# Kernel tuning notes

Measured on AMD Instinct MI355X. Metric: run time of the kernel, lower is better.

The kernel has to match this reference:

```python
import jax, jax.numpy as jnp
import numpy as np

B, S, D = 8, 1024, 1024
H, DK = 16, 64  # heads, key_size (== head_size)
NEG = 1e12


def setup_inputs() -> dict:
    key = jax.random.key(0)
    ks = jax.random.split(key, 10)
    s = 1.0 / np.sqrt(D)
    return {
        "q": jax.random.normal(ks[0], (B, S, D), jnp.float32),
        "k": jax.random.normal(ks[1], (B, S, D), jnp.float32),
        "v": jax.random.normal(ks[2], (B, S, D), jnp.float32),
        "pos_bias": jax.random.normal(ks[3], (S, S, DK), jnp.float32) * 0.02,
        "Wq": jax.random.normal(ks[4], (D, H * DK), jnp.float32) * s,
        "Wk": jax.random.normal(ks[5], (D, H * DK), jnp.float32) * s,
        "Wv": jax.random.normal(ks[6], (D, H * DK), jnp.float32) * s,
        "Wo": jax.random.normal(ks[7], (H * DK, D), jnp.float32) * s,
        "bq": jnp.zeros((H * DK,), jnp.float32),
        "bk": jnp.zeros((H * DK,), jnp.float32),
        "bv": jnp.zeros((H * DK,), jnp.float32),
        "bo": jnp.zeros((D,), jnp.float32),
        "q_mask": jnp.ones((B, S), jnp.int32),
        "v_mask": jnp.ones((B, S), jnp.int32),
    }


def reference(q, k, v, pos_bias, Wq, Wk, Wv, Wo, bq, bk, bv, bo, q_mask, v_mask):
    qm = q_mask.astype(q.dtype)  # [B,Sq]
    vm = v_mask.astype(q.dtype)  # [B,Sk]
    # Projections (faithful quirk: K is projected from v, as in the source)
    qw = (q @ Wq + bq).reshape(B, S, H, DK)
    kw = (v @ Wk + bk).reshape(B, S, H, DK)
    vw = (v @ Wv + bv).reshape(B, S, H, DK)
    # scores + inline relative-position bias ('typial_relative' branch)
    a = jnp.einsum('bjhd,bkhd->bhjk', qw, kw)
    a = a + jnp.einsum('bjhd,jkd->bhjk', qw, pos_bias)
    a = a / jnp.sqrt(jnp.asarray(DK, a.dtype))
    # additive key mask, then softmax over keys
    a = a - (1.0 - vm)[:, None, None, :] * NEG
    a = jax.nn.softmax(a, axis=-1)
    o = jnp.einsum('bhjk,bkhd->bjhd', a, vw)  # [B,Sq,H,DK]
    o = o.reshape(B, S, H * DK) @ Wo + bo
    # multiplicative query mask on output
    o = o * qm[:, :, None]
    return o
```

## Files before the change

kernel.cpp:

```cpp
#include <hip/hip_runtime.h>

using short8 = __attribute__((ext_vector_type(8))) short;
using f32x4  = __attribute__((ext_vector_type(4))) float;
using u16x4  = __attribute__((ext_vector_type(4))) unsigned short;
using fl4    = __attribute__((ext_vector_type(4))) float;

#define MFMA16(a, b, c) __builtin_amdgcn_mfma_f32_16x16x32_bf16((a), (b), (c), 0, 0, 0)

static __device__ __forceinline__ unsigned short f2bf(float f) {
  union { float f; unsigned u; } x; x.f = f;
  return (unsigned short)((x.u + 0x7FFFu + ((x.u >> 16) & 1u)) >> 16);
}
static __device__ __forceinline__ float bf2f(unsigned short s) {
  union { unsigned u; float f; } x; x.u = ((unsigned)s) << 16;
  return x.f;
}
static __device__ __forceinline__ float fexp2(float x) {
  float r; asm("v_exp_f32 %0, %1" : "=v"(r) : "v"(x)); return r;
}
static __device__ __forceinline__ unsigned pk2(float lo, float hi) {
  unsigned r; asm("v_cvt_pk_bf16_f32 %0, %1, %2" : "=v"(r) : "v"(lo), "v"(hi));
  return r;
}

static __device__ __forceinline__ void gload16(const void* g, void* l) {
  __builtin_amdgcn_global_load_lds((const __attribute__((address_space(1))) void*)g,
                                   (__attribute__((address_space(3))) void*)l, 16, 0, 0);
}

#define LOG2E 1.4426950408889634f

__global__ __launch_bounds__(256) void k_wconv4(
    const float* __restrict__ W0, const float* __restrict__ W1,
    const float* __restrict__ W2, const float* __restrict__ W3,
    unsigned short* __restrict__ Wt0, unsigned short* __restrict__ Wt1,
    unsigned short* __restrict__ Wt2, unsigned short* __restrict__ Wt3) {
  const float* W = (blockIdx.z == 0) ? W0 : (blockIdx.z == 1) ? W1
                   : (blockIdx.z == 2) ? W2 : W3;
  unsigned short* Wt = (blockIdx.z == 0) ? Wt0 : (blockIdx.z == 1) ? Wt1
                       : (blockIdx.z == 2) ? Wt2 : Wt3;
  __shared__ float tile[64][65];
  const int t = threadIdx.x;
  const int n0 = blockIdx.x * 64, k0 = blockIdx.y * 64;
#pragma unroll
  for (int p = 0; p < 4; ++p) {
    int row = p * 16 + (t >> 4);
    int c4 = (t & 15) * 4;
    fl4 val = *(const fl4*)&W[(size_t)(k0 + row) * 1024 + n0 + c4];
    tile[row][c4 + 0] = val[0];
    tile[row][c4 + 1] = val[1];
    tile[row][c4 + 2] = val[2];
    tile[row][c4 + 3] = val[3];
  }
  __syncthreads();
#pragma unroll
  for (int p = 0; p < 4; ++p) {
    int n = p * 16 + (t >> 4);
    int k4 = (t & 15) * 4;
    u16x4 u;
    u[0] = f2bf(tile[k4 + 0][n]);
    u[1] = f2bf(tile[k4 + 1][n]);
    u[2] = f2bf(tile[k4 + 2][n]);
    u[3] = f2bf(tile[k4 + 3][n]);
    *(u16x4*)&Wt[(size_t)(n0 + n) * 1024 + k0 + k4] = u;
  }
}

__global__ __launch_bounds__(256) void k_cvt(const float* __restrict__ a,
                                             const float* __restrict__ b,
                                             unsigned short* __restrict__ oa,
                                             unsigned short* __restrict__ ob) {
  const float* src = blockIdx.y ? b : a;
  unsigned short* dst = blockIdx.y ? ob : oa;
  size_t i = ((size_t)blockIdx.x * 256 + threadIdx.x) * 8;
  fl4 v0 = *(const fl4*)&src[i];
  fl4 v1 = *(const fl4*)&src[i + 4];
  u16x4 u0, u1;
  u0[0] = f2bf(v0[0]); u0[1] = f2bf(v0[1]); u0[2] = f2bf(v0[2]); u0[3] = f2bf(v0[3]);
  u1[0] = f2bf(v1[0]); u1[1] = f2bf(v1[1]); u1[2] = f2bf(v1[2]); u1[3] = f2bf(v1[3]);
  *(u16x4*)&dst[i] = u0;
  *(u16x4*)&dst[i + 4] = u1;
}

#define GEMM3_CORE(APTR, BPTR)                                                  \
  const int t = threadIdx.x, lane = t & 63, w = t >> 6;                         \
  const int g = lane >> 4, ln = lane & 15;                                      \
  const int wm = w >> 1, wn = w & 1;                                            \
  __shared__ unsigned short sh[24576];    \
  const int srow = lane >> 2;                                                   \
  const int sc = (lane & 3) ^ ((lane >> 3) & 3);                                \
  const int rsw = ((ln >> 1) & 3);                                              \
  f32x4 acc[4][4] = {};                                                         \
  _Pragma("unroll") for (int pre = 0; pre < 2; ++pre) {                         \
    _Pragma("unroll") for (int p = 0; p < 2; ++p) {                             \
      gload16(&APTR[(size_t)(m0 + p * 64 + w * 16 + srow) * 1024 + pre * 32 + sc * 8], \
              &sh[pre * 8192 + (p * 64 + w * 16) * 32]);                        \
      gload16(&BPTR[(size_t)(n0 + p * 64 + w * 16 + srow) * 1024 + pre * 32 + sc * 8], \
              &sh[pre * 8192 + 4096 + (p * 64 + w * 16) * 32]);                 \
    }                                                                           \
  }                                                                             \
  int cur = 0;                                                                  \
  for (int tt = 0; tt < 32; ++tt) {                                             \
    if (tt < 31) {                                                              \
      asm volatile("s_waitcnt vmcnt(4)" ::: "memory");                          \
    } else {                                                                    \
      asm volatile("s_waitcnt vmcnt(0)" ::: "memory");                          \
    }                                                                           \
    __builtin_amdgcn_sched_barrier(0);                                          \
    __builtin_amdgcn_s_barrier();                                               \
    __builtin_amdgcn_sched_barrier(0);                                          \
    if (tt < 30) {                                                              \
      int bb = cur + 2; if (bb >= 3) bb -= 3;                                   \
      int kk = (tt + 2) * 32;                                                   \
      _Pragma("unroll") for (int p = 0; p < 2; ++p) {                           \
        gload16(&APTR[(size_t)(m0 + p * 64 + w * 16 + srow) * 1024 + kk + sc * 8], \
                &sh[bb * 8192 + (p * 64 + w * 16) * 32]);                       \
        gload16(&BPTR[(size_t)(n0 + p * 64 + w * 16 + srow) * 1024 + kk + sc * 8], \
                &sh[bb * 8192 + 4096 + (p * 64 + w * 16) * 32]);                \
      }                                                                         \
    }                                                                           \
    const unsigned short* As = &sh[cur * 8192];                                 \
    const unsigned short* Bs = As + 4096;                                       \
    short8 af[4], bfr[4];                                                       \
    _Pragma("unroll") for (int fm = 0; fm < 4; ++fm)                            \
        af[fm] = *(const short8*)&As[(wm * 64 + fm * 16 + ln) * 32 + (g ^ rsw) * 8]; \
    _Pragma("unroll") for (int fn = 0; fn < 4; ++fn)                            \
        bfr[fn] = *(const short8*)&Bs[(wn * 64 + fn * 16 + ln) * 32 + (g ^ rsw) * 8]; \
    _Pragma("unroll") for (int fn = 0; fn < 4; ++fn) {                          \
      _Pragma("unroll") for (int fm = 0; fm < 4; ++fm)                          \
          acc[fm][fn] = MFMA16(af[fm], bfr[fn], acc[fm][fn]);                   \
    }                                                                           \
    cur = (cur == 2) ? 0 : cur + 1;                                             \
  }

__global__ __launch_bounds__(256) void k_proj3(
    const unsigned short* __restrict__ QB, const unsigned short* __restrict__ VB,
    const unsigned short* __restrict__ WtQ, const unsigned short* __restrict__ WtK,
    const unsigned short* __restrict__ WtV,
    const float* __restrict__ bq, const float* __restrict__ bk,
    const float* __restrict__ bv,
    unsigned short* __restrict__ QW, unsigned short* __restrict__ KW,
    unsigned short* __restrict__ VWT) {
  const int mode = blockIdx.z;
  const unsigned short* A8 = (mode == 0) ? QB : VB;
  const unsigned short* Wt = (mode == 0) ? WtQ : (mode == 1) ? WtK : WtV;
  const float* bias = (mode == 0) ? bq : (mode == 1) ? bk : bv;
  const int n0 = blockIdx.x * 128, m0 = blockIdx.y * 128;
  GEMM3_CORE(A8, Wt)
  __syncthreads();
  const float scale = (mode == 0) ? (0.125f * LOG2E) : 1.0f;
#pragma unroll
  for (int fn = 0; fn < 4; ++fn) {
    float bn = bias[n0 + wn * 64 + fn * 16 + ln];
#pragma unroll
    for (int fm = 0; fm < 4; ++fm) {
#pragma unroll
      for (int r = 0; r < 4; ++r) {
        float val = (acc[fm][fn][r] + bn) * scale;
        sh[(wm * 64 + fm * 16 + 4 * g + r) * 132 + wn * 64 + fn * 16 + ln] = f2bf(val);
      }
    }
  }
  __syncthreads();
  if (mode < 2) {
    unsigned short* OUT = (mode == 0) ? QW : KW;
#pragma unroll
    for (int p = 0; p < 16; ++p) {
      int row = p * 8 + (t >> 5), c4 = (t & 31) * 4;
      *(u16x4*)&OUT[(size_t)(m0 + row) * 1024 + n0 + c4] =
          *(const u16x4*)&sh[row * 132 + c4];
    }
  } else {
    const int b = m0 >> 10, s0 = m0 & 1023;
#pragma unroll
    for (int p = 0; p < 16; ++p) {
#pragma unroll
      for (int qh = 0; qh < 2; ++qh) {
        int hdl = p * 8 + (t >> 5);
        int sl = qh * 64 + (t & 31) * 2;
        unsigned lo = sh[sl * 132 + hdl];
        unsigned hi = sh[(sl + 1) * 132 + hdl];
        int hd = n0 + hdl;
        int h = hd >> 6, d = hd & 63;
        *(unsigned*)&VWT[((size_t)(b * 16 + h) * 64 + d) * 1024 + s0 + sl] =
            lo | (hi << 16);
      }
    }
  }
}

__global__ __launch_bounds__(256) void k_out3(
    const unsigned short* __restrict__ OB, const unsigned short* __restrict__ WtO,
    const float* __restrict__ bo, const int* __restrict__ qmask,
    float* __restrict__ out) {
  const int n0 = blockIdx.x * 128, m0 = blockIdx.y * 128;
  GEMM3_CORE(OB, WtO)
  float bn[4];
#pragma unroll
  for (int fn = 0; fn < 4; ++fn) bn[fn] = bo[n0 + wn * 64 + fn * 16 + ln];
#pragma unroll
  for (int fm = 0; fm < 4; ++fm) {
#pragma unroll
    for (int r = 0; r < 4; ++r) {
      int row = m0 + wm * 64 + fm * 16 + 4 * g + r;
      float qm = (float)qmask[row];
#pragma unroll
      for (int fn = 0; fn < 4; ++fn)
        out[(size_t)row * 1024 + n0 + wn * 64 + fn * 16 + ln] =
            (acc[fm][fn][r] + bn[fn]) * qm;
    }
  }
}

__global__ __launch_bounds__(256) void k_pbias(
    const unsigned short* __restrict__ QW, const float* __restrict__ pb,
    const int* __restrict__ vmask, unsigned short* __restrict__ CB, int jbase) {
  const int kt = blockIdx.x;
  const int jl = blockIdx.y;
  const int j = jbase + jl;
  const int t = threadIdx.x, lane = t & 63, w = t >> 6;
  const int g = lane >> 4, ln = lane & 15;
  const int wm = w >> 1, wn = w & 1;
  __shared__ unsigned short sm[18432];
  unsigned short* a_lds = sm;
  unsigned short* b_lds = sm + 9216;
#pragma unroll
  for (int p = 0; p < 8; ++p) {
    int i4 = p * 256 + t;
    int row = i4 >> 4, c4 = (i4 & 15) * 4;
    *(u16x4*)&a_lds[row * 72 + c4] =
        *(const u16x4*)&QW[((size_t)(row >> 4) * 1024 + j) * 1024 + (row & 15) * 64 + c4];
  }
#pragma unroll
  for (int p = 0; p < 8; ++p) {
    int i4 = p * 256 + t;
    int row = i4 >> 4, c4 = (i4 & 15) * 4;
    fl4 val = *(const fl4*)&pb[((size_t)j * 1024 + kt * 128 + row) * 64 + c4];
    u16x4 u;
    u[0] = f2bf(val[0]); u[1] = f2bf(val[1]);
    u[2] = f2bf(val[2]); u[3] = f2bf(val[3]);
    *(u16x4*)&b_lds[row * 72 + c4] = u;
  }
  __syncthreads();
  f32x4 acc[4][4] = {};
#pragma unroll
  for (int ks = 0; ks < 2; ++ks) {
    short8 af[4];
#pragma unroll
    for (int fm = 0; fm < 4; ++fm)
      af[fm] = *(const short8*)&a_lds[(wm * 64 + fm * 16 + ln) * 72 + ks * 32 + 8 * g];
#pragma unroll
    for (int fn = 0; fn < 4; ++fn) {
      short8 bfr = *(const short8*)&b_lds[(wn * 64 + fn * 16 + ln) * 72 + ks * 32 + 8 * g];
#pragma unroll
      for (int fm = 0; fm < 4; ++fm) acc[fm][fn] = MFMA16(af[fm], bfr, acc[fm][fn]);
    }
  }
  __syncthreads();
#pragma unroll
  for (int fn = 0; fn < 4; ++fn) {
    int kcol = kt * 128 + wn * 64 + fn * 16 + ln;
#pragma unroll
    for (int fm = 0; fm < 4; ++fm) {
      float off = vmask[(wm * 4 + fm) * 1024 + kcol] ? 0.f : (-1e12f * LOG2E);
#pragma unroll
      for (int r = 0; r < 4; ++r)
        sm[(wm * 64 + fm * 16 + 4 * g + r) * 132 + wn * 64 + fn * 16 + ln] =
            f2bf(acc[fm][fn][r] + off);
    }
  }
  __syncthreads();
#pragma unroll
  for (int p = 0; p < 16; ++p) {
    int row = p * 8 + (t >> 5), c4 = (t & 31) * 4;
    *(u16x4*)&CB[((size_t)row * 512 + jl) * 1024 + kt * 128 + c4] =
        *(const u16x4*)&sm[row * 132 + c4];
  }
}

__global__ __launch_bounds__(256) void k_attn(
    const unsigned short* __restrict__ QW, const unsigned short* __restrict__ KW,
    const unsigned short* __restrict__ VWT, const unsigned short* __restrict__ CB,
    unsigned short* __restrict__ OB, int jbase) {
  const int B = blockIdx.x;
  const int wrk = (B & 7) * 128 + (B >> 3);
  const int jt = wrk & 7, h = (wrk >> 3) & 15, b = wrk >> 7;
  const int t = threadIdx.x, lane = t & 63, w = t >> 6;
  const int g = lane >> 4, ln = lane & 15;
  const int j0 = jbase + jt * 64;
  const int jl0 = jt * 64;
  __shared__ unsigned short lds_k[128 * 72];
  __shared__ unsigned short lds_vt[64 * 136];
  __shared__ unsigned short lds_p[4 * 16 * 136];
  unsigned short* pw = &lds_p[w * (16 * 136)];
  short8 qf[2];
  {
    const size_t qrow = ((size_t)b * 1024 + (j0 + w * 16 + ln)) * 1024 + h * 64;
    qf[0] = *(const short8*)&QW[qrow + 8 * g];
    qf[1] = *(const short8*)&QW[qrow + 32 + 8 * g];
  }
  const size_t cb_row = ((size_t)(b * 16 + h) * 512 + jl0 + w * 16 + ln) * 1024;

  u16x4 rk[8], rv[8], rcb[8];
#define LOAD_KV(kt_)                                                              \
  {                                                                               \
    _Pragma("unroll") for (int p = 0; p < 8; ++p) {                               \
      int i4 = p * 256 + t;                                                       \
      int row = i4 >> 4, c4 = (i4 & 15) * 4;                                      \
      rk[p] = *(const u16x4*)&KW[((size_t)b * 1024 + (kt_) * 128 + row) * 1024 +  \
                                 h * 64 + c4];                                    \
    }                                                                             \
    _Pragma("unroll") for (int p = 0; p < 8; ++p) {                               \
      int i4 = p * 256 + t;                                                       \
      int row = i4 >> 5, c4 = (i4 & 31) * 4;                                      \
      rv[p] = *(const u16x4*)&VWT[(((size_t)b * 16 + h) * 64 + row) * 1024 +      \
                                  (kt_) * 128 + c4];                              \
    }                                                                             \
    _Pragma("unroll") for (int p = 0; p < 8; ++p)                                 \
        rcb[p] = *(const u16x4*)&CB[cb_row + (kt_) * 128 + p * 16 + 4 * g];       \
  }

  LOAD_KV(0);
  f32x4 o_acc[4] = {};
  float l_par = 0.f;

  for (int kt = 0; kt < 8; ++kt) {
    __syncthreads();
#pragma unroll
    for (int p = 0; p < 8; ++p) {
      int i4 = p * 256 + t;
      int row = i4 >> 4, c4 = (i4 & 15) * 4;
      *(u16x4*)&lds_k[row * 72 + c4] = rk[p];
    }
#pragma unroll
    for (int p = 0; p < 8; ++p) {
      int i4 = p * 256 + t;
      int row = i4 >> 5, c4 = (i4 & 31) * 4;
      *(u16x4*)&lds_vt[row * 136 + c4] = rv[p];
    }
    f32x4 s[8];
#pragma unroll
    for (int fm = 0; fm < 8; ++fm) {
#pragma unroll
      for (int r = 0; r < 4; ++r) s[fm][r] = bf2f(rcb[fm][r]);
    }
    if (kt < 7) LOAD_KV(kt + 1);
    __syncthreads();
#pragma unroll
    for (int ks = 0; ks < 2; ++ks) {
#pragma unroll
      for (int fm = 0; fm < 8; ++fm) {
        short8 af = *(const short8*)&lds_k[(fm * 16 + ln) * 72 + ks * 32 + 8 * g];
        s[fm] = MFMA16(af, qf[ks], s[fm]);
      }
    }
#pragma unroll
    for (int fm = 0; fm < 8; ++fm) {
      float pv0 = fexp2(s[fm][0] - 17.0f);
      float pv1 = fexp2(s[fm][1] - 17.0f);
      float pv2 = fexp2(s[fm][2] - 17.0f);
      float pv3 = fexp2(s[fm][3] - 17.0f);
      l_par += (pv0 + pv1) + (pv2 + pv3);
      union { u16x4 v; unsigned u[2]; } pp;
      pp.u[0] = pk2(pv0, pv1);
      pp.u[1] = pk2(pv2, pv3);
      *(u16x4*)&pw[ln * 136 + fm * 16 + 4 * g] = pp.v;
    }
    asm volatile("s_waitcnt lgkmcnt(0)" ::: "memory");
#pragma unroll
    for (int ks = 0; ks < 4; ++ks) {
      short8 bp = *(const short8*)&pw[ln * 136 + ks * 32 + 8 * g];
#pragma unroll
      for (int fm = 0; fm < 4; ++fm) {
        short8 av = *(const short8*)&lds_vt[(fm * 16 + ln) * 136 + ks * 32 + 8 * g];
        o_acc[fm] = MFMA16(av, bp, o_acc[fm]);
      }
    }
  }
  l_par += __shfl_xor(l_par, 16);
  l_par += __shfl_xor(l_par, 32);
  float inv = 1.0f / l_par;
  const size_t orow = ((size_t)b * 1024 + (j0 + w * 16 + ln)) * 1024 + h * 64;
#pragma unroll
  for (int fm = 0; fm < 4; ++fm) {
    union { u16x4 v; unsigned u[2]; } uo;
    uo.u[0] = pk2(o_acc[fm][0] * inv, o_acc[fm][1] * inv);
    uo.u[1] = pk2(o_acc[fm][2] * inv, o_acc[fm][3] * inv);
    *(u16x4*)&OB[orow + fm * 16 + 4 * g] = uo.v;
  }
#undef LOAD_KV
}

extern "C" void kernel_launch(void* const* d_in, const int* in_sizes, int n_in,
                              void* d_out, int out_size, void* d_ws, size_t ws_size,
                              hipStream_t stream) {
  const float* q  = (const float*)d_in[0];
  const float* v  = (const float*)d_in[2];
  const float* pb = (const float*)d_in[3];
  const float* Wq = (const float*)d_in[4];
  const float* Wk = (const float*)d_in[5];
  const float* Wv = (const float*)d_in[6];
  const float* Wo = (const float*)d_in[7];
  const float* bq = (const float*)d_in[8];
  const float* bk = (const float*)d_in[9];
  const float* bv = (const float*)d_in[10];
  const float* bo = (const float*)d_in[11];
  const int* qm = (const int*)d_in[12];
  const int* vm = (const int*)d_in[13];
  float* out = (float*)d_out;

  unsigned short* ws = (unsigned short*)d_ws;
  const size_t M1 = 1024 * 1024;
  unsigned short* WTQ = ws;
  unsigned short* WTK = WTQ + M1;
  unsigned short* WTV = WTK + M1;
  unsigned short* WTO = WTV + M1;
  unsigned short* QB  = WTO + M1;
  unsigned short* VB  = QB + 8 * M1;
  unsigned short* QW  = VB + 8 * M1;
  unsigned short* KW  = QW + 8 * M1;
  unsigned short* VWT = KW + 8 * M1;
  unsigned short* OB  = VWT + 8 * M1;
  unsigned short* CB  = OB + 8 * M1;

  k_wconv4<<<dim3(16, 16, 4), 256, 0, stream>>>(Wq, Wk, Wv, Wo, WTQ, WTK, WTV, WTO);
  k_cvt<<<dim3(4096, 2), 256, 0, stream>>>(q, v, QB, VB);
  k_proj3<<<dim3(8, 64, 3), 256, 0, stream>>>(QB, VB, WTQ, WTK, WTV, bq, bk, bv,
                                              QW, KW, VWT);
  for (int st = 0; st < 2; ++st) {
    k_pbias<<<dim3(8, 512), 256, 0, stream>>>(QW, pb, vm, CB, st * 512);
    k_attn<<<dim3(1024), 256, 0, stream>>>(QW, KW, VWT, CB, OB, st * 512);
  }
  k_out3<<<dim3(8, 64), 256, 0, stream>>>(OB, WTO, bo, qm, out);
}
```

Before: 377.6 us.

## Transpose P in registers with permlane swaps instead of LDS round-trip

Removes the per-wave LDS staging buffer for the softmax probabilities. P fragments now go straight from the QK^T MFMA output layout into the PV MFMA operand layout using v_permlane32/16_swap, with the exp computation interleaved per k-step. Also adds s_setprio around the MFMA blocks and raises the occupancy hint in launch_bounds to 4 blocks. This cuts LDS traffic and the lgkmcnt wait, but the permlane mapping has to match the operand layout exactly or the results are wrong, and the occupancy hint may cause register spills.

```diff
diff --git a/kernel.cpp b/kernel.cpp
--- a/kernel.cpp
+++ b/kernel.cpp
@@ -278,7 +278,7 @@
   }
 }
 
-__global__ __launch_bounds__(256) void k_attn(
+__global__ __launch_bounds__(256, 4) void k_attn(
     const unsigned short* __restrict__ QW, const unsigned short* __restrict__ KW,
     const unsigned short* __restrict__ VWT, const unsigned short* __restrict__ CB,
     unsigned short* __restrict__ OB, int jbase) {
@@ -291,8 +291,6 @@
   const int jl0 = jt * 64;
   __shared__ unsigned short lds_k[128 * 72];
   __shared__ unsigned short lds_vt[64 * 136];
-  __shared__ unsigned short lds_p[4 * 16 * 136];
-  unsigned short* pw = &lds_p[w * (16 * 136)];
   short8 qf[2];
   {
     const size_t qrow = ((size_t)b * 1024 + (j0 + w * 16 + ln)) * 1024 + h * 64;
@@ -346,6 +344,7 @@
     }
     if (kt < 7) LOAD_KV(kt + 1);
     __syncthreads();
+    __builtin_amdgcn_s_setprio(1);
 #pragma unroll
     for (int ks = 0; ks < 2; ++ks) {
 #pragma unroll
@@ -354,27 +353,30 @@
         s[fm] = MFMA16(af, qf[ks], s[fm]);
       }
     }
-#pragma unroll
-    for (int fm = 0; fm < 8; ++fm) {
-      float pv0 = fexp2(s[fm][0] - 17.0f);
-      float pv1 = fexp2(s[fm][1] - 17.0f);
-      float pv2 = fexp2(s[fm][2] - 17.0f);
-      float pv3 = fexp2(s[fm][3] - 17.0f);
-      l_par += (pv0 + pv1) + (pv2 + pv3);
-      union { u16x4 v; unsigned u[2]; } pp;
-      pp.u[0] = pk2(pv0, pv1);
-      pp.u[1] = pk2(pv2, pv3);
-      *(u16x4*)&pw[ln * 136 + fm * 16 + 4 * g] = pp.v;
-    }
-    asm volatile("s_waitcnt lgkmcnt(0)" ::: "memory");
+    __builtin_amdgcn_s_setprio(0);
 #pragma unroll
     for (int ks = 0; ks < 4; ++ks) {
-      short8 bp = *(const short8*)&pw[ln * 136 + ks * 32 + 8 * g];
+      const int fA = 2 * ks, fB = 2 * ks + 1;
+      float eA0 = fexp2(s[fA][0] - 17.0f), eA1 = fexp2(s[fA][1] - 17.0f);
+      float eA2 = fexp2(s[fA][2] - 17.0f), eA3 = fexp2(s[fA][3] - 17.0f);
+      float eB0 = fexp2(s[fB][0] - 17.0f), eB1 = fexp2(s[fB][1] - 17.0f);
+      float eB2 = fexp2(s[fB][2] - 17.0f), eB3 = fexp2(s[fB][3] - 17.0f);
+      l_par += ((eA0 + eA1) + (eA2 + eA3)) + ((eB0 + eB1) + (eB2 + eB3));
+      unsigned a0 = pk2(eA0, eA1), a1 = pk2(eA2, eA3);
+      unsigned b0 = pk2(eB0, eB1), b1 = pk2(eB2, eB3);
+      asm("v_permlane32_swap_b32 %0, %1" : "+v"(a0), "+v"(b0));
+      asm("v_permlane16_swap_b32 %0, %1" : "+v"(a0), "+v"(b0));
+      asm("v_permlane32_swap_b32 %0, %1" : "+v"(a1), "+v"(b1));
+      asm("v_permlane16_swap_b32 %0, %1" : "+v"(a1), "+v"(b1));
+      union { short8 v; unsigned u[4]; } bp;
+      bp.u[0] = a0; bp.u[1] = a1; bp.u[2] = b0; bp.u[3] = b1;
+      __builtin_amdgcn_s_setprio(1);
 #pragma unroll
       for (int fm = 0; fm < 4; ++fm) {
         short8 av = *(const short8*)&lds_vt[(fm * 16 + ln) * 136 + ks * 32 + 8 * g];
-        o_acc[fm] = MFMA16(av, bp, o_acc[fm]);
+        o_acc[fm] = MFMA16(av, bp.v, o_acc[fm]);
       }
+      __builtin_amdgcn_s_setprio(0);
     }
   }
   l_par += __shfl_xor(l_par, 16);
```

Result: slower. 509.9 us (+35.0%).
